# Kernel optimization log

Measured on AMD Instinct MI355X. Metric: run time of the kernel, lower is better.

Reference implementation:

```python
import jax, jax.numpy as jnp
import numpy as np

B, S = 32, 2048
DIM_ACTION = 32
DIM_STRUCT = 64
HIDDEN = 128  # mlp_hidden_dim default = dim_action * 4
EPS = 1e-12   # F.normalize eps


def l2norm(t):
    n = jnp.linalg.norm(t, axis=-1, keepdims=True)
    return t / jnp.maximum(n, EPS)


def setup_inputs() -> dict:
    key = jax.random.key(0)
    ks = jax.random.split(key, 9)
    sd = lambda fan_in: 1.0 / np.sqrt(fan_in)
    inp = {
        "actions": jax.random.normal(ks[0], (B, S, DIM_ACTION), dtype=jnp.float32),
        # MLP: dim_action -> hidden -> hidden -> dim_structure^2 (depth=2 hidden relu layers)
        "w0": jax.random.uniform(ks[1], (DIM_ACTION, HIDDEN), jnp.float32, -sd(DIM_ACTION), sd(DIM_ACTION)),
        "b0": jnp.zeros((HIDDEN,), jnp.float32),
        "w1": jax.random.uniform(ks[2], (HIDDEN, HIDDEN), jnp.float32, -sd(HIDDEN), sd(HIDDEN)),
        "b1": jnp.zeros((HIDDEN,), jnp.float32),
        "w2": jax.random.uniform(ks[3], (HIDDEN, DIM_STRUCT * DIM_STRUCT), jnp.float32, -sd(HIDDEN), sd(HIDDEN)),
        "b2": jnp.zeros((DIM_STRUCT * DIM_STRUCT,), jnp.float32),
        # RNN init hidden parameter [1, dim_structure], ~N(0, 0.01)
        "init_hidden": jax.random.normal(ks[4], (1, DIM_STRUCT), dtype=jnp.float32) * 0.01,
    }
    return inp


def reference(actions, w0, b0, w1, b1, w2, b2, init_hidden):
    # MLP to transitions: [B, S, d*d]
    h = jax.nn.relu(jnp.einsum("bsa,ah->bsh", actions, w0) + b0)
    h = jax.nn.relu(jnp.einsum("bsh,hk->bsk", h, w1) + b1)
    t = jnp.einsum("bsh,ho->bso", h, w2) + b2
    transitions = t.reshape(B, S, DIM_STRUCT, DIM_STRUCT)  # [B, S, i, j]

    # RNN: hidden_{t+1} = l2norm(relu(hidden_t @ T_t)), scanned over seq
    hidden0 = jnp.broadcast_to(l2norm(init_hidden), (B, DIM_STRUCT))

    def step(hidden, trans):  # trans: [B, i, j]
        hidden = jnp.einsum("bi,bij->bj", hidden, trans)
        hidden = l2norm(jax.nn.relu(hidden))
        return hidden, hidden

    trans_seq = jnp.swapaxes(transitions, 0, 1)  # [S, B, i, j]
    _, hiddens = jax.lax.scan(step, hidden0, trans_seq)  # [S, B, d]
    return jnp.swapaxes(hiddens, 0, 1)  # [B, S, d]
```

## Files before the change

### kernel.cpp

```cpp
#include <hip/hip_runtime.h>

#define B_ 32
#define S_ 2048
#define DA 32
#define DH 128
#define DS 64
#define DS2 4096
#define TKK 16

template <int CTRL>
__device__ __forceinline__ float dpp_add(float x) {
  int t = __builtin_amdgcn_update_dpp(0, __float_as_int(x), CTRL, 0xF, 0xF, true);
  return x + __int_as_float(t);
}
__device__ __forceinline__ float row_sum16(float x) {
  x = dpp_add<0xB1>(x);
  x = dpp_add<0x4E>(x);
  x = dpp_add<0x141>(x);
  x = dpp_add<0x140>(x);
  return x;
}

__device__ __forceinline__ void gl2lds16(const float* g, float* l) {
  __builtin_amdgcn_global_load_lds(
      (const __attribute__((address_space(1))) void*)g,
      (__attribute__((address_space(3))) void*)l, 16, 0, 0);
}

struct SharedRnn {
  float4 ring[6][16][64];
  int flags[6];
  int cons;
};
struct SharedGemm {
  float As[2][TKK][128];
  float4 part[256][17];
};
struct SharedMlp {
  float a_t[DA][64];
  float w0_l[DA][DH];
  float h0t[DH][64];
};
union SharedU {
  SharedRnn r;
  SharedGemm g;
  SharedMlp m;
};

__device__ __forceinline__ void mlp_tile(
    const float* __restrict__ actions, const float* __restrict__ w0,
    const float* __restrict__ b0, const float* __restrict__ w1,
    const float* __restrict__ b1, float* __restrict__ h1t,
    int s_base, int M, int m0, SharedMlp& sm, int tid)
{
  {
    int tok = tid >> 3, kq = tid & 7;
    int tl = m0 + tok;
    int b = tl & 31, s = s_base + (tl >> 5);
    float4 v = *(const float4*)(actions + ((size_t)b * S_ + s) * DA + 4 * kq);
    sm.a_t[4 * kq + 0][tok] = v.x; sm.a_t[4 * kq + 1][tok] = v.y;
    sm.a_t[4 * kq + 2][tok] = v.z; sm.a_t[4 * kq + 3][tok] = v.w;
  }
#pragma unroll
  for (int q = 0; q < 2; ++q) {
    int g = tid + 512 * q;
    ((float4*)&sm.w0_l[0][0])[g] = ((const float4*)w0)[g];
  }
  __syncthreads();

  const int tm = tid & 15;
  const int tn = tid >> 4;

  float acc[4][4];
#pragma unroll
  for (int mi = 0; mi < 4; ++mi)
#pragma unroll
    for (int ni = 0; ni < 4; ++ni) acc[mi][ni] = 0.f;

#pragma unroll 4
  for (int k = 0; k < DA; ++k) {
    float4 a4 = *(const float4*)&sm.a_t[k][4 * tm];
    float4 w4 = *(const float4*)&sm.w0_l[k][4 * tn];
    float av[4] = {a4.x, a4.y, a4.z, a4.w};
    float wv[4] = {w4.x, w4.y, w4.z, w4.w};
#pragma unroll
    for (int mi = 0; mi < 4; ++mi)
#pragma unroll
      for (int ni = 0; ni < 4; ++ni) acc[mi][ni] += av[mi] * wv[ni];
  }
  {
    float4 b4 = *(const float4*)(b0 + 4 * tn);
    float bv[4] = {b4.x, b4.y, b4.z, b4.w};
#pragma unroll
    for (int mi = 0; mi < 4; ++mi)
#pragma unroll
      for (int ni = 0; ni < 4; ++ni)
        sm.h0t[4 * tn + ni][4 * tm + mi] = fmaxf(acc[mi][ni] + bv[ni], 0.f);
  }
  __syncthreads();

  float acc1[4][4];
#pragma unroll
  for (int mi = 0; mi < 4; ++mi)
#pragma unroll
    for (int ni = 0; ni < 4; ++ni) acc1[mi][ni] = 0.f;

#pragma unroll 4
  for (int k = 0; k < DH; ++k) {
    float4 h4 = *(const float4*)&sm.h0t[k][4 * tm];
    float4 w4 = *(const float4*)(w1 + (size_t)k * DH + 4 * tn);
    float av[4] = {h4.x, h4.y, h4.z, h4.w};
    float wv[4] = {w4.x, w4.y, w4.z, w4.w};
#pragma unroll
    for (int mi = 0; mi < 4; ++mi)
#pragma unroll
      for (int ni = 0; ni < 4; ++ni) acc1[mi][ni] += av[mi] * wv[ni];
  }
  {
    float4 b4 = *(const float4*)(b1 + 4 * tn);
    float bv[4] = {b4.x, b4.y, b4.z, b4.w};
#pragma unroll
    for (int ni = 0; ni < 4; ++ni) {
      float4 o;
      o.x = fmaxf(acc1[0][ni] + bv[ni], 0.f);
      o.y = fmaxf(acc1[1][ni] + bv[ni], 0.f);
      o.z = fmaxf(acc1[2][ni] + bv[ni], 0.f);
      o.w = fmaxf(acc1[3][ni] + bv[ni], 0.f);
      *(float4*)(h1t + (size_t)(4 * tn + ni) * M + m0 + 4 * tm) = o;
    }
  }
}

__device__ __forceinline__ void trans_tile(
    const float* __restrict__ h1t, const float* __restrict__ w2,
    const float* __restrict__ b2, float* __restrict__ trans,
    int M, int n0, int m0, SharedGemm& sg, int tid)
{
  const int w  = tid >> 6;
  const int lw = tid & 63;

  auto aload = [&](int t, int buf) {
    const int kr = 2 * w + (lw >> 5);
    const int c4 = 4 * (lw & 31);
    gl2lds16(h1t + (size_t)(t * TKK + kr) * M + m0 + c4, &sg.As[buf][2 * w][0]);
  };

  aload(0, 0);

  const int sub = tid & 255;
  const int khalf = tid >> 8;
  const int mg = sub >> 4;
  const int ng = sub & 15;
  float acc[8][8];
#pragma unroll
  for (int mi = 0; mi < 8; ++mi)
#pragma unroll
    for (int ni = 0; ni < 8; ++ni) acc[mi][ni] = 0.f;

  int buf = 0;
  const int kb = 8 * khalf;
  const float* w2p = w2 + n0 + 4 * ng + (size_t)kb * DS2;
  for (int t = 0; t < DH / TKK; ++t) {
    __syncthreads();
    if (t < DH / TKK - 1) aload(t + 1, buf ^ 1);
    const float* w2k = w2p + (size_t)t * TKK * DS2;
#pragma unroll
    for (int k8 = 0; k8 < 8; ++k8) {
      const int k = kb + k8;
      float4 b0v = *(const float4*)(w2k + (size_t)k8 * DS2);
      float4 b1v = *(const float4*)(w2k + (size_t)k8 * DS2 + 64);
      float4 a0 = *(const float4*)&sg.As[buf][k][8 * mg];
      float4 a1 = *(const float4*)&sg.As[buf][k][8 * mg + 4];
      float av[8] = {a0.x, a0.y, a0.z, a0.w, a1.x, a1.y, a1.z, a1.w};
      float bv[8] = {b0v.x, b0v.y, b0v.z, b0v.w, b1v.x, b1v.y, b1v.z, b1v.w};
#pragma unroll
      for (int mi = 0; mi < 8; ++mi)
#pragma unroll
        for (int ni = 0; ni < 8; ++ni) acc[mi][ni] += av[mi] * bv[ni];
    }
    buf ^= 1;
  }

  __syncthreads();
  if (khalf) {
#pragma unroll
    for (int mi = 0; mi < 8; ++mi) {
      sg.part[sub][2 * mi] =
          make_float4(acc[mi][0], acc[mi][1], acc[mi][2], acc[mi][3]);
      sg.part[sub][2 * mi + 1] =
          make_float4(acc[mi][4], acc[mi][5], acc[mi][6], acc[mi][7]);
    }
  }
  __syncthreads();
  if (!khalf) {
    float4 bb0 = *(const float4*)(b2 + n0 + 4 * ng);
    float4 bb1 = *(const float4*)(b2 + n0 + 64 + 4 * ng);
    float bv[8] = {bb0.x, bb0.y, bb0.z, bb0.w, bb1.x, bb1.y, bb1.z, bb1.w};
#pragma unroll
    for (int mi = 0; mi < 8; ++mi) {
      float4 p0 = sg.part[sub][2 * mi];
      float4 p1 = sg.part[sub][2 * mi + 1];
      float pv[8] = {p0.x, p0.y, p0.z, p0.w, p1.x, p1.y, p1.z, p1.w};
      float* dst = trans + (size_t)(m0 + 8 * mg + mi) * DS2 + n0;
#pragma unroll
      for (int q = 0; q < 2; ++q) {
        float4 o;
        o.x = acc[mi][4 * q + 0] + pv[4 * q + 0] + bv[4 * q + 0];
        o.y = acc[mi][4 * q + 1] + pv[4 * q + 1] + bv[4 * q + 1];
        o.z = acc[mi][4 * q + 2] + pv[4 * q + 2] + bv[4 * q + 2];
        o.w = acc[mi][4 * q + 3] + pv[4 * q + 3] + bv[4 * q + 3];
        *(float4*)(dst + 64 * q + 4 * ng) = o;
      }
    }
  }
}

__global__ __launch_bounds__(512) void k_mlp01(
    const float* __restrict__ actions, const float* __restrict__ w0,
    const float* __restrict__ b0, const float* __restrict__ w1,
    const float* __restrict__ b1, float* __restrict__ h1t,
    int s_base, int M)
{
  __shared__ SharedMlp sm;
  mlp_tile(actions, w0, b0, w1, b1, h1t, s_base, M, blockIdx.x * 64, sm,
           threadIdx.x);
}

__global__ __launch_bounds__(512, 1) void k_comb(
    const float* __restrict__ actions, const float* __restrict__ w0,
    const float* __restrict__ b0, const float* __restrict__ w1,
    const float* __restrict__ b1, const float* __restrict__ w2,
    const float* __restrict__ b2, const float* __restrict__ init_hidden,
    float* __restrict__ trans0, float* __restrict__ trans1,
    float* __restrict__ h1t0, float* __restrict__ h1t1,
    float* __restrict__ hstate, float* __restrict__ out,
    int c, int SC, int nch)
{
  __shared__ SharedU sh;
  const int tid = threadIdx.x;
  const int M = SC * 32;

  if (blockIdx.x >= 32) {
    const int bi = blockIdx.x - 32;
    if (c < nch) {
      const float* h1t = (c & 1) ? h1t1 : h1t0;
      float* trans = (c & 1) ? trans1 : trans0;
      const int NJ = (M / 128) * (DS2 / 128);
      for (int j = bi; j < NJ; j += 224) {
        const int mt = j >> 5, nt = j & 31;
        trans_tile(h1t, w2, b2, trans, M, nt * 128, mt * 128, sh.g, tid);
        __syncthreads();
      }
      if (c + 1 < nch) {
        __syncthreads();
        float* h1n = ((c + 1) & 1) ? h1t1 : h1t0;
        for (int j = bi; j < M / 64; j += 224) {
          mlp_tile(actions, w0, b0, w1, b1, h1n, (c + 1) * SC, M, j * 64,
                   sh.m, tid);
          __syncthreads();
        }
      }
    }
    return;
  }

  if (c == 0) return;
  const int cc = c - 1;
  const float* trans = (cc & 1) ? trans1 : trans0;
  const int s_base = cc * SC;
  const int wv = tid >> 6;
  const int lane = tid & 63;
  const int b = blockIdx.x;

  if (tid < 6) sh.r.flags[tid] = 0;
  if (tid == 6) sh.r.cons = 0;
  __syncthreads();

  const float* base = trans + (size_t)b * DS2;

  if (wv > 0) {
    if (wv <= 3) {
      const int p = wv - 1;
      int prev = -1;
      for (int s = p; s < SC; s += 3) {
        while (s - __hip_atomic_load(&sh.r.cons, __ATOMIC_RELAXED,
                                     __HIP_MEMORY_SCOPE_WORKGROUP) > 5)
          __builtin_amdgcn_s_sleep(2);
        const int slot = s % 6;
        const float* g = base + (size_t)s * (32 * DS2) + 4 * lane;
        float* l = (float*)&sh.r.ring[slot][0][0];
#pragma unroll
        for (int q = 0; q < 16; ++q)
          gl2lds16(g + q * 256, l + q * 256);
        if (prev >= 0) {
          asm volatile("s_waitcnt vmcnt(16)" ::: "memory");
          __hip_atomic_store(&sh.r.flags[prev % 6], prev + 1, __ATOMIC_RELAXED,
                             __HIP_MEMORY_SCOPE_WORKGROUP);
        }
        prev = s;
      }
      if (prev >= 0) {
        asm volatile("s_waitcnt vmcnt(0)" ::: "memory");
        __hip_atomic_store(&sh.r.flags[prev % 6], prev + 1, __ATOMIC_RELAXED,
                           __HIP_MEMORY_SCOPE_WORKGROUP);
      }
    }
  } else {
    const int d = lane >> 4;
    const int cq = lane & 15;
    const bool d1 = (d & 1), d2 = (d & 2);
    const int pb = lane & 48;

    float4 hq;
    if (cc == 0) {
      hq = *(const float4*)(init_hidden + 4 * cq);
      float ss0 = row_sum16(hq.x * hq.x + hq.y * hq.y + hq.z * hq.z + hq.w * hq.w);
      float iv0 = 1.0f / fmaxf(sqrtf(ss0), 1e-12f);
      hq.x *= iv0; hq.y *= iv0; hq.z *= iv0; hq.w *= iv0;
    } else {
      hq = *(const float4*)(hstate + b * DS + 4 * cq);
    }
    float inv_prev = 1.0f;

    float* outp = out + ((size_t)b * S_ + s_base) * DS + 4 * cq;
    int fpre = -1;
    for (int s = 0; s < SC; ++s) {
      const int slot = s % 6;
      if (fpre < s + 1) {
        while (__hip_atomic_load(&sh.r.flags[slot], __ATOMIC_ACQUIRE,
                                 __HIP_MEMORY_SCOPE_WORKGROUP) < s + 1)
          __builtin_amdgcn_s_sleep(0);
      }
      fpre = __hip_atomic_load(&sh.r.flags[(s + 1) % 6], __ATOMIC_ACQUIRE,
                               __HIP_MEMORY_SCOPE_WORKGROUP);

      float hsel = d2 ? (d1 ? hq.w : hq.z) : (d1 ? hq.y : hq.x);
      float ax = 0.f, ay = 0.f, az = 0.f, aw = 0.f;
#pragma unroll
      for (int q = 0; q < 16; ++q) {
        float4 t4 = sh.r.ring[slot][q][lane];
        float hb = __shfl(hsel, pb + q, 64);
        ax += hb * t4.x; ay += hb * t4.y;
        az += hb * t4.z; aw += hb * t4.w;
      }
      __hip_atomic_store(&sh.r.cons, s + 1, __ATOMIC_RELAXED,
                         __HIP_MEMORY_SCOPE_WORKGROUP);

      ax += __shfl_xor(ax, 16, 64); ax += __shfl_xor(ax, 32, 64);
      ay += __shfl_xor(ay, 16, 64); ay += __shfl_xor(ay, 32, 64);
      az += __shfl_xor(az, 16, 64); az += __shfl_xor(az, 32, 64);
      aw += __shfl_xor(aw, 16, 64); aw += __shfl_xor(aw, 32, 64);
      hq.x = fmaxf(ax * inv_prev, 0.f);
      hq.y = fmaxf(ay * inv_prev, 0.f);
      hq.z = fmaxf(az * inv_prev, 0.f);
      hq.w = fmaxf(aw * inv_prev, 0.f);
      float ss = row_sum16(hq.x * hq.x + hq.y * hq.y + hq.z * hq.z + hq.w * hq.w);
      float inv = 1.0f / fmaxf(sqrtf(ss), 1e-12f);
      if (d == 0) {
        float4 o;
        o.x = hq.x * inv; o.y = hq.y * inv; o.z = hq.z * inv; o.w = hq.w * inv;
        *(float4*)(outp + (size_t)s * DS) = o;
      }
      inv_prev = inv;
    }
    if (d == 0) {
      float4 o;
      o.x = hq.x * inv_prev; o.y = hq.y * inv_prev;
      o.z = hq.z * inv_prev; o.w = hq.w * inv_prev;
      *(float4*)(hstate + b * DS + 4 * cq) = o;
    }
  }
}

extern "C" void kernel_launch(void* const* d_in, const int* in_sizes, int n_in,
                              void* d_out, int out_size, void* d_ws, size_t ws_size,
                              hipStream_t stream) {
  const float* actions     = (const float*)d_in[0];
  const float* w0          = (const float*)d_in[1];
  const float* b0          = (const float*)d_in[2];
  const float* w1          = (const float*)d_in[3];
  const float* b1          = (const float*)d_in[4];
  const float* w2          = (const float*)d_in[5];
  const float* b2          = (const float*)d_in[6];
  const float* init_hidden = (const float*)d_in[7];
  float* out = (float*)d_out;

  int SC = 2048;
  while (SC > 4) {
    size_t need = 2 * ((size_t)SC * 32 * DS2 * 4 + (size_t)SC * 32 * DH * 4)
                + (size_t)B_ * DS * 4;
    if (need <= ws_size) break;
    SC >>= 1;
  }
  float* trans0 = (float*)d_ws;
  float* trans1 = trans0 + (size_t)SC * 32 * DS2;
  float* h1t0   = trans1 + (size_t)SC * 32 * DS2;
  float* h1t1   = h1t0 + (size_t)SC * 32 * DH;
  float* hstate = h1t1 + (size_t)SC * 32 * DH;

  const int M = SC * 32;
  const int nch = S_ / SC;

  hipLaunchKernelGGL(k_mlp01, dim3(M / 64), dim3(512), 0, stream,
                     actions, w0, b0, w1, b1, h1t0, 0, M);
  for (int c = 0; c <= nch; ++c) {
    hipLaunchKernelGGL(k_comb, dim3(256), dim3(512), 0, stream,
                       actions, w0, b0, w1, b1, w2, b2, init_hidden,
                       trans0, trans1, h1t0, h1t1, hstate, out, c, SC, nch);
  }
}
```

Measured before the change: 1.754 ms.

## Stage full K panel in LDS and prefetch next tile during epilogue

The transition GEMM tile now loads the whole 128-row A panel into LDS at once, replacing the double-buffered 16-row chunks. This removes the per-k-step barriers, and each half of the block covers a contiguous 64-wide K range. The next tile's A panel is issued with async global-to-LDS loads while the split-K reduction and output stores run, so the load overlaps the epilogue. In exchange, LDS use grows to roughly 134KB for the GEMM union member, and correctness now depends on explicit vmcnt waits.

```diff
diff --git a/kernel.cpp b/kernel.cpp
--- a/kernel.cpp
+++ b/kernel.cpp
@@ -33,7 +33,7 @@
   int cons;
 };
 struct SharedGemm {
-  float As[2][TKK][128];
+  float As[DH][128];
   float4 part[256][17];
 };
 struct SharedMlp {
@@ -131,46 +131,54 @@
   }
 }
 
-__device__ __forceinline__ void trans_tile(
+__device__ __forceinline__ void trans_loop(
     const float* __restrict__ h1t, const float* __restrict__ w2,
     const float* __restrict__ b2, float* __restrict__ trans,
-    int M, int n0, int m0, SharedGemm& sg, int tid)
+    int M, int bi, SharedGemm& sg, int tid)
 {
   const int w  = tid >> 6;
   const int lw = tid & 63;
-
-  auto aload = [&](int t, int buf) {
-    const int kr = 2 * w + (lw >> 5);
+  const int NJ = (M / 128) * (DS2 / 128);
+  if (bi >= NJ) return;
+
+  auto aloadF = [&](int j) {
+    const int m0 = (j >> 5) * 128;
+    const int rb = 16 * w;
     const int c4 = 4 * (lw & 31);
-    gl2lds16(h1t + (size_t)(t * TKK + kr) * M + m0 + c4, &sg.As[buf][2 * w][0]);
+    const int ro = lw >> 5;
+#pragma unroll
+    for (int q = 0; q < 8; ++q) {
+      const int kr = rb + 2 * q + ro;
+      gl2lds16(h1t + (size_t)kr * M + m0 + c4, &sg.As[rb + 2 * q][0]);
+    }
   };
-
-  aload(0, 0);
 
   const int sub = tid & 255;
   const int khalf = tid >> 8;
   const int mg = sub >> 4;
   const int ng = sub & 15;
-  float acc[8][8];
-#pragma unroll
-  for (int mi = 0; mi < 8; ++mi)
-#pragma unroll
-    for (int ni = 0; ni < 8; ++ni) acc[mi][ni] = 0.f;
-
-  int buf = 0;
-  const int kb = 8 * khalf;
-  const float* w2p = w2 + n0 + 4 * ng + (size_t)kb * DS2;
-  for (int t = 0; t < DH / TKK; ++t) {
-    __syncthreads();
-    if (t < DH / TKK - 1) aload(t + 1, buf ^ 1);
-    const float* w2k = w2p + (size_t)t * TKK * DS2;
-#pragma unroll
-    for (int k8 = 0; k8 < 8; ++k8) {
-      const int k = kb + k8;
-      float4 b0v = *(const float4*)(w2k + (size_t)k8 * DS2);
-      float4 b1v = *(const float4*)(w2k + (size_t)k8 * DS2 + 64);
-      float4 a0 = *(const float4*)&sg.As[buf][k][8 * mg];
-      float4 a1 = *(const float4*)&sg.As[buf][k][8 * mg + 4];
+  const int kb = 64 * khalf;
+
+  aloadF(bi);
+  asm volatile("s_waitcnt vmcnt(0)" ::: "memory");
+  __syncthreads();
+
+  for (int j = bi; j < NJ; j += 224) {
+    const int m0 = (j >> 5) * 128, n0 = (j & 31) * 128;
+
+    float acc[8][8];
+#pragma unroll
+    for (int mi = 0; mi < 8; ++mi)
+#pragma unroll
+      for (int ni = 0; ni < 8; ++ni) acc[mi][ni] = 0.f;
+
+    const float* w2p = w2 + (size_t)kb * DS2 + n0 + 4 * ng;
+#pragma unroll 4
+    for (int k8 = 0; k8 < 64; ++k8) {
+      float4 b0v = *(const float4*)(w2p + (size_t)k8 * DS2);
+      float4 b1v = *(const float4*)(w2p + (size_t)k8 * DS2 + 64);
+      float4 a0 = *(const float4*)&sg.As[kb + k8][8 * mg];
+      float4 a1 = *(const float4*)&sg.As[kb + k8][8 * mg + 4];
       float av[8] = {a0.x, a0.y, a0.z, a0.w, a1.x, a1.y, a1.z, a1.w};
       float bv[8] = {b0v.x, b0v.y, b0v.z, b0v.w, b1v.x, b1v.y, b1v.z, b1v.w};
 #pragma unroll
@@ -178,40 +186,43 @@
 #pragma unroll
         for (int ni = 0; ni < 8; ++ni) acc[mi][ni] += av[mi] * bv[ni];
     }
-    buf ^= 1;
-  }
-
-  __syncthreads();
-  if (khalf) {
-#pragma unroll
-    for (int mi = 0; mi < 8; ++mi) {
-      sg.part[sub][2 * mi] =
-          make_float4(acc[mi][0], acc[mi][1], acc[mi][2], acc[mi][3]);
-      sg.part[sub][2 * mi + 1] =
-          make_float4(acc[mi][4], acc[mi][5], acc[mi][6], acc[mi][7]);
-    }
-  }
-  __syncthreads();
-  if (!khalf) {
-    float4 bb0 = *(const float4*)(b2 + n0 + 4 * ng);
-    float4 bb1 = *(const float4*)(b2 + n0 + 64 + 4 * ng);
-    float bv[8] = {bb0.x, bb0.y, bb0.z, bb0.w, bb1.x, bb1.y, bb1.z, bb1.w};
-#pragma unroll
-    for (int mi = 0; mi < 8; ++mi) {
-      float4 p0 = sg.part[sub][2 * mi];
-      float4 p1 = sg.part[sub][2 * mi + 1];
-      float pv[8] = {p0.x, p0.y, p0.z, p0.w, p1.x, p1.y, p1.z, p1.w};
-      float* dst = trans + (size_t)(m0 + 8 * mg + mi) * DS2 + n0;
-#pragma unroll
-      for (int q = 0; q < 2; ++q) {
-        float4 o;
-        o.x = acc[mi][4 * q + 0] + pv[4 * q + 0] + bv[4 * q + 0];
-        o.y = acc[mi][4 * q + 1] + pv[4 * q + 1] + bv[4 * q + 1];
-        o.z = acc[mi][4 * q + 2] + pv[4 * q + 2] + bv[4 * q + 2];
-        o.w = acc[mi][4 * q + 3] + pv[4 * q + 3] + bv[4 * q + 3];
-        *(float4*)(dst + 64 * q + 4 * ng) = o;
-      }
-    }
+    __syncthreads();
+
+    if (khalf) {
+#pragma unroll
+      for (int mi = 0; mi < 8; ++mi) {
+        sg.part[sub][2 * mi] =
+            make_float4(acc[mi][0], acc[mi][1], acc[mi][2], acc[mi][3]);
+        sg.part[sub][2 * mi + 1] =
+            make_float4(acc[mi][4], acc[mi][5], acc[mi][6], acc[mi][7]);
+      }
+    }
+    if (j + 224 < NJ) aloadF(j + 224);
+    __syncthreads();
+
+    if (!khalf) {
+      float4 bb0 = *(const float4*)(b2 + n0 + 4 * ng);
+      float4 bb1 = *(const float4*)(b2 + n0 + 64 + 4 * ng);
+      float bv[8] = {bb0.x, bb0.y, bb0.z, bb0.w, bb1.x, bb1.y, bb1.z, bb1.w};
+#pragma unroll
+      for (int mi = 0; mi < 8; ++mi) {
+        float4 p0 = sg.part[sub][2 * mi];
+        float4 p1 = sg.part[sub][2 * mi + 1];
+        float pv[8] = {p0.x, p0.y, p0.z, p0.w, p1.x, p1.y, p1.z, p1.w};
+        float* dst = trans + (size_t)(m0 + 8 * mg + mi) * DS2 + n0;
+#pragma unroll
+        for (int q = 0; q < 2; ++q) {
+          float4 o;
+          o.x = acc[mi][4 * q + 0] + pv[4 * q + 0] + bv[4 * q + 0];
+          o.y = acc[mi][4 * q + 1] + pv[4 * q + 1] + bv[4 * q + 1];
+          o.z = acc[mi][4 * q + 2] + pv[4 * q + 2] + bv[4 * q + 2];
+          o.w = acc[mi][4 * q + 3] + pv[4 * q + 3] + bv[4 * q + 3];
+          *(float4*)(dst + 64 * q + 4 * ng) = o;
+        }
+      }
+    }
+    asm volatile("s_waitcnt vmcnt(0)" ::: "memory");
+    __syncthreads();
   }
 }
 
@@ -245,12 +256,7 @@
     if (c < nch) {
       const float* h1t = (c & 1) ? h1t1 : h1t0;
       float* trans = (c & 1) ? trans1 : trans0;
-      const int NJ = (M / 128) * (DS2 / 128);
-      for (int j = bi; j < NJ; j += 224) {
-        const int mt = j >> 5, nt = j & 31;
-        trans_tile(h1t, w2, b2, trans, M, nt * 128, mt * 128, sh.g, tid);
-        __syncthreads();
-      }
+      trans_loop(h1t, w2, b2, trans, M, bi, sh.g, tid);
       if (c + 1 < nch) {
         __syncthreads();
         float* h1n = ((c + 1) & 1) ? h1t1 : h1t0;
```

Measured after the change: 1.586 ms. 9.6% less time.
